# Optimization experiments

Measured on AMD Instinct MI355X. Metric: run time of the kernel, lower is better.

Reference implementation:

```python
import jax, jax.numpy as jnp
import numpy as np

B, K, D, H, A = 8192, 10, 64, 128, 16
E = K * (K - 1)
# lexicographic ordered pairs (i,j), i != j -- matches adj.nonzero() and sorted(Dict.keys())
_PAIRS = np.array([(i, j) for i in range(K) for j in range(K) if i != j], dtype=np.int32)
SRC = jnp.asarray(_PAIRS[:, 0])  # message for edge (i,j) is aggregated at node i (row)
DST = jnp.asarray(_PAIRS[:, 1])


def setup_inputs() -> dict:
    key = jax.random.key(0)
    k1, k2, k3, k4, k5, k6 = jax.random.split(key, 6)
    F = D + H + A  # node MLP input dim
    return {
        "states": jax.random.normal(k1, (B, K, D), jnp.float32),
        "action_vec": jax.random.normal(k2, (B, K, A), jnp.float32),
        # one Linear(2D -> H) per ordered pair, stacked [E, 2D, H]
        "W_edge": jax.random.normal(k3, (E, 2 * D, H), jnp.float32) * (1.0 / np.sqrt(2 * D)),
        "b_edge": jax.random.normal(k4, (E, H), jnp.float32) * 0.01,
        # one Linear(D+H+A -> D) per node, stacked [K, F, D]
        "W_node": jax.random.normal(k5, (K, F, D), jnp.float32) * (1.0 / np.sqrt(F)),
        "b_node": jax.random.normal(k6, (K, D), jnp.float32) * 0.01,
    }


def reference(states, action_vec, W_edge, b_edge, W_node, b_node):
    # states: [B,K,D], action_vec: [B,K,A]
    b, k, d = states.shape
    # gather endpoints per ordered edge: [B,E,2D]
    pair_feat = jnp.concatenate([states[:, SRC, :], states[:, DST, :]], axis=-1)
    # per-edge-type Linear + tanh, batched as one grouped GEMM: [B,E,H]
    msg = jnp.tanh(jnp.einsum('bef,efh->beh', pair_feat, W_edge) + b_edge)
    # unsorted_segment_sum over source node index (row): [B,K,H]
    agg = jnp.zeros((b, k, msg.shape[-1]), msg.dtype).at[:, SRC, :].add(msg)
    # node input: [x, action, agg] -> per-node Linear + tanh: [B,K,D]
    node_in = jnp.concatenate([states, action_vec, agg], axis=-1)
    out = jnp.tanh(jnp.einsum('bkf,kfd->bkd', node_in, W_node) + b_node)
    return out
```

## Files before the change

### kernel.cpp

```cpp
#include <hip/hip_runtime.h>

typedef _Float16 f16;
typedef _Float16 f16x4 __attribute__((ext_vector_type(4)));
typedef _Float16 f16x8 __attribute__((ext_vector_type(8)));
typedef float    f32x4 __attribute__((ext_vector_type(4)));

#define Kn   10
#define En   90
#define BM   128
#define WE_ELEMS (90*128*128)

__device__ __forceinline__ float fast_exp2(float x){
#if __has_builtin(__builtin_amdgcn_exp2f)
    return __builtin_amdgcn_exp2f(x);
#else
    return exp2f(x);
#endif
}
__device__ __forceinline__ float fast_rcp(float x){
#if __has_builtin(__builtin_amdgcn_rcpf)
    return __builtin_amdgcn_rcpf(x);
#else
    return 1.0f/x;
#endif
}
__device__ __forceinline__ float tanh_fast(float x){
    float e = fast_exp2(x * 2.88539008177792681472f);
    return 1.0f - 2.0f * fast_rcp(e + 1.0f);
}

__global__ void we_transpose(const float* __restrict__ We, f16* __restrict__ out){
    int gid = blockIdx.x*256 + threadIdx.x;
    int e  = gid >> 11;
    int r  = gid & 2047;
    int h  = r & 127;
    int f0 = (r >> 7) << 3;
    const float* src = We + e*16384 + h;
    f16x8 v;
    #pragma unroll
    for (int k=0;k<8;k++) v[k] = (f16)src[(f0+k)*128];
    *(f16x8*)(out + e*16384 + h*128 + f0) = v;
}

__global__ void wn_transpose(const float* __restrict__ Wn, f16* __restrict__ out){
    int gid = blockIdx.x*256 + threadIdx.x;
    int k = gid / 14336;
    int r = gid - k*14336;
    int d = r / 224;
    int f = r - d*224;
    float v = (f < 208) ? Wn[k*13312 + f*64 + d] : 0.0f;
    out[gid] = (f16)v;
}

__launch_bounds__(256, 2)
__global__ void gnn_main(const float* __restrict__ states,
                         const float* __restrict__ action,
                         const float* __restrict__ b_edge,
                         const float* __restrict__ b_node,
                         const f16*  __restrict__ We_t,
                         const f16*  __restrict__ Wn_t,
                         float* __restrict__ out)
{
    __shared__ alignas(16) f16 S[9216 + 9216 + 19456];
    f16* sAi = S;
    f16* sAj = S + 9216;
    f16* sWU = S + 18432;

    const int t    = threadIdx.x;
    const int b0   = blockIdx.x * BM;
    const int i    = blockIdx.y;
    const int lane = t & 63;
    const int wid  = t >> 6;
    const int l15  = lane & 15;
    const int q    = lane >> 4;
    const int qo   = q << 3;
    const int wr = (wid >> 1) * 64;
    const int wc = (wid & 1) * 64;

    #pragma unroll
    for (int it=0; it<8; ++it){
        int cid = it*256 + t;
        int row = cid >> 4;
        int c4  = (cid & 15) << 2;
        const float4 v = *(const float4*)(states + (b0+row)*640 + i*64 + c4);
        f16x4 hv; hv[0]=(f16)v.x; hv[1]=(f16)v.y; hv[2]=(f16)v.z; hv[3]=(f16)v.w;
        *(f16x4*)(sAi + row*72 + c4) = hv;
    }

    f32x4 agg[4][4] = {};

    #pragma unroll 1
    for (int et=0; et<9; ++et){
        const int j = et + (et >= i);
        const int e = 9*i + et;

        #pragma unroll
        for (int it=0; it<8; ++it){
            int cid = it*256 + t;
            int row = cid >> 4;
            int c4  = (cid & 15) << 2;
            const float4 v = *(const float4*)(states + (b0+row)*640 + j*64 + c4);
            f16x4 hv; hv[0]=(f16)v.x; hv[1]=(f16)v.y; hv[2]=(f16)v.z; hv[3]=(f16)v.w;
            *(f16x4*)(sAj + row*72 + c4) = hv;
        }
        const f16* wsrc = We_t + e*16384;
        #pragma unroll
        for (int it=0; it<8; ++it){
            int cid = it*256 + t;
            int h   = cid >> 4;
            int c8  = (cid & 15) << 3;
            *(f16x8*)(sWU + h*136 + c8) = *(const f16x8*)(wsrc + h*128 + c8);
        }
        __syncthreads();

        f32x4 msg[4][4] = {};
        #pragma unroll
        for (int ks=0; ks<4; ++ks){
            const f16* ab = (ks<2) ? (sAi + ks*32) : (sAj + (ks-2)*32);
            f16x8 af[4], bf[4];
            #pragma unroll
            for (int rt=0; rt<4; ++rt)
                af[rt] = *(const f16x8*)(ab + (wr + rt*16 + l15)*72 + qo);
            #pragma unroll
            for (int c=0; c<4; ++c)
                bf[c] = *(const f16x8*)(sWU + (wc + c*16 + l15)*136 + ks*32 + qo);
            #pragma unroll
            for (int rt=0; rt<4; ++rt)
                #pragma unroll
                for (int c=0; c<4; ++c)
                    msg[rt][c] = __builtin_amdgcn_mfma_f32_16x16x32_f16(af[rt], bf[c], msg[rt][c], 0,0,0);
        }
        float bias[4];
        #pragma unroll
        for (int c=0;c<4;c++) bias[c] = b_edge[e*128 + wc + c*16 + l15];
        #pragma unroll
        for (int rt=0; rt<4; ++rt)
            #pragma unroll
            for (int c=0;c<4;c++)
                #pragma unroll
                for (int r2=0;r2<4;r2++)
                    agg[rt][c][r2] += tanh_fast(msg[rt][c][r2] + bias[c]);
        __syncthreads();
    }

    #pragma unroll
    for (int rt=0; rt<4; ++rt)
        #pragma unroll
        for (int c=0;c<4;c++)
            #pragma unroll
            for (int r2=0;r2<4;r2++){
                int row = wr + rt*16 + q*4 + r2;
                int col = wc + c*16 + l15;
                sWU[row*152 + col] = (f16)agg[rt][c][r2];
            }
    {
        int row = t >> 1, c0 = 128 + ((t & 1) << 3);
        f16x8 z; 
        #pragma unroll
        for (int k=0;k<8;k++) z[k] = (f16)0.0f;
        *(f16x8*)(sWU + row*152 + c0) = z;
    }
    #pragma unroll
    for (int it=0; it<2; ++it){
        int cid = it*256 + t;
        int row = cid >> 2;
        int c4  = (cid & 3) << 2;
        const float4 v = *(const float4*)(action + (b0+row)*160 + i*16 + c4);
        f16x4 hv; hv[0]=(f16)v.x; hv[1]=(f16)v.y; hv[2]=(f16)v.z; hv[3]=(f16)v.w;
        *(f16x4*)(sAj + row*72 + c4) = hv;
    }
    __syncthreads();

    f32x4 acc[2][4] = {};
    const f16* wn = Wn_t + i*14336;
    #pragma unroll
    for (int ks=0; ks<7; ++ks){
        int kk = ks*32 + qo;
        f16x8 af[2], bf[4];
        #pragma unroll
        for (int rt=0; rt<2; ++rt){
            int row = wid*32 + rt*16 + l15;
            const f16* ap = (kk < 64) ? (sAi + row*72 + kk)
                          : (kk < 80) ? (sAj + row*72 + (kk-64))
                                      : (sWU + row*152 + (kk-80));
            af[rt] = *(const f16x8*)ap;
        }
        #pragma unroll
        for (int c=0;c<4;c++)
            bf[c] = *(const f16x8*)(wn + (c*16 + l15)*224 + kk);
        #pragma unroll
        for (int rt=0; rt<2; ++rt)
            #pragma unroll
            for (int c=0;c<4;c++)
                acc[rt][c] = __builtin_amdgcn_mfma_f32_16x16x32_f16(af[rt], bf[c], acc[rt][c], 0,0,0);
    }
    float bn[4];
    #pragma unroll
    for (int c=0;c<4;c++) bn[c] = b_node[i*64 + c*16 + l15];
    #pragma unroll
    for (int rt=0; rt<2; ++rt)
        #pragma unroll
        for (int c=0;c<4;c++)
            #pragma unroll
            for (int r2=0;r2<4;r2++){
                int row = wid*32 + rt*16 + q*4 + r2;
                int col = c*16 + l15;
                out[((b0+row)*10 + i)*64 + col] = tanh_fast(acc[rt][c][r2] + bn[c]);
            }
}

extern "C" void kernel_launch(void* const* d_in, const int* in_sizes, int n_in,
                              void* d_out, int out_size, void* d_ws, size_t ws_size,
                              hipStream_t stream) {
    const float* states = (const float*)d_in[0];
    const float* action = (const float*)d_in[1];
    const float* W_edge = (const float*)d_in[2];
    const float* b_edge = (const float*)d_in[3];
    const float* W_node = (const float*)d_in[4];
    const float* b_node = (const float*)d_in[5];
    f16* We_t = (f16*)d_ws;
    f16* Wn_t = We_t + WE_ELEMS;

    hipLaunchKernelGGL(we_transpose, dim3(720), dim3(256), 0, stream, W_edge, We_t);
    hipLaunchKernelGGL(wn_transpose, dim3(560), dim3(256), 0, stream, W_node, Wn_t);
    hipLaunchKernelGGL(gnn_main, dim3(8192/BM, Kn), dim3(256), 0, stream,
                       states, action, b_edge, b_node, We_t, Wn_t, (float*)d_out);
}
```

Baseline: 157.7 us.

## Pre-convert inputs to fp16, stream via global_load_lds with swizzled double-buffered LDS

A single prep kernel converts states and action to fp16, pre-swizzles edge and node weights into MFMA fragment order, and pre-scales biases by the tanh exponent constant. The main kernel loads state tiles directly into LDS with global_load_lds, double-buffers the neighbour tile, and uses an XOR swizzle instead of padded rows. Edge weights are read straight from global memory into registers in fragment order, so the weight staging through LDS goes away. The tanh accumulation is rewritten with folded constants, adding +9 at the end. The extra full-array fp16 conversion pass adds memory traffic, and a third occupancy target may add register pressure.

```diff
diff --git a/kernel.cpp b/kernel.cpp
--- a/kernel.cpp
+++ b/kernel.cpp
@@ -5,10 +5,13 @@
 typedef _Float16 f16x8 __attribute__((ext_vector_type(8)));
 typedef float    f32x4 __attribute__((ext_vector_type(4)));
 
-#define Kn   10
-#define En   90
-#define BM   128
-#define WE_ELEMS (90*128*128)
+#define S2C 2.88539008177792681472f
+
+#define OFF_ST16 0u
+#define OFF_AC16 5242880u
+#define OFF_WEF  6553600u
+#define OFF_WNF  8028160u
+#define OFF_BE2  8171520u
 
 __device__ __forceinline__ float fast_exp2(float x){
 #if __has_builtin(__builtin_amdgcn_exp2f)
@@ -24,155 +27,168 @@
     return 1.0f/x;
 #endif
 }
-__device__ __forceinline__ float tanh_fast(float x){
-    float e = fast_exp2(x * 2.88539008177792681472f);
-    return 1.0f - 2.0f * fast_rcp(e + 1.0f);
-}
-
-__global__ void we_transpose(const float* __restrict__ We, f16* __restrict__ out){
-    int gid = blockIdx.x*256 + threadIdx.x;
-    int e  = gid >> 11;
-    int r  = gid & 2047;
-    int h  = r & 127;
-    int f0 = (r >> 7) << 3;
-    const float* src = We + e*16384 + h;
-    f16x8 v;
-    #pragma unroll
-    for (int k=0;k<8;k++) v[k] = (f16)src[(f0+k)*128];
-    *(f16x8*)(out + e*16384 + h*128 + f0) = v;
-}
-
-__global__ void wn_transpose(const float* __restrict__ Wn, f16* __restrict__ out){
-    int gid = blockIdx.x*256 + threadIdx.x;
-    int k = gid / 14336;
-    int r = gid - k*14336;
-    int d = r / 224;
-    int f = r - d*224;
-    float v = (f < 208) ? Wn[k*13312 + f*64 + d] : 0.0f;
-    out[gid] = (f16)v;
-}
-
-__launch_bounds__(256, 2)
-__global__ void gnn_main(const float* __restrict__ states,
-                         const float* __restrict__ action,
-                         const float* __restrict__ b_edge,
-                         const float* __restrict__ b_node,
-                         const f16*  __restrict__ We_t,
-                         const f16*  __restrict__ Wn_t,
-                         float* __restrict__ out)
-{
-    __shared__ alignas(16) f16 S[9216 + 9216 + 19456];
-    f16* sAi = S;
-    f16* sAj = S + 9216;
-    f16* sWU = S + 18432;
-
-    const int t    = threadIdx.x;
-    const int b0   = blockIdx.x * BM;
-    const int i    = blockIdx.y;
-    const int lane = t & 63;
-    const int wid  = t >> 6;
-    const int l15  = lane & 15;
-    const int q    = lane >> 4;
-    const int qo   = q << 3;
-    const int wr = (wid >> 1) * 64;
-    const int wc = (wid & 1) * 64;
-
-    #pragma unroll
-    for (int it=0; it<8; ++it){
-        int cid = it*256 + t;
-        int row = cid >> 4;
-        int c4  = (cid & 15) << 2;
-        const float4 v = *(const float4*)(states + (b0+row)*640 + i*64 + c4);
-        f16x4 hv; hv[0]=(f16)v.x; hv[1]=(f16)v.y; hv[2]=(f16)v.z; hv[3]=(f16)v.w;
-        *(f16x4*)(sAi + row*72 + c4) = hv;
-    }
+
+__device__ __forceinline__ void gl_lds16(const f16* g, f16* l){
+    __builtin_amdgcn_global_load_lds(
+        (const __attribute__((address_space(1))) unsigned int*)g,
+        (__attribute__((address_space(3))) unsigned int*)l, 16, 0, 0);
+}
+
+#define MFMA16(a,b,c) __builtin_amdgcn_mfma_f32_16x16x32_f16(a,b,c,0,0,0)
+
+__global__ void prep(const float* __restrict__ st, const float* __restrict__ ac,
+                     const float* __restrict__ We, const float* __restrict__ be,
+                     const float* __restrict__ Wn, const float* __restrict__ bn,
+                     f16* __restrict__ ws16){
+    const int bid = blockIdx.x, t = threadIdx.x;
+    if (bid < 5120){
+        int g = bid*256 + t;
+        const float4 v = ((const float4*)st)[g];
+        f16x4 h; h[0]=(f16)v.x; h[1]=(f16)v.y; h[2]=(f16)v.z; h[3]=(f16)v.w;
+        *(f16x4*)(ws16 + OFF_ST16 + (size_t)g*4) = h;
+    } else if (bid < 6400){
+        int g = (bid-5120)*256 + t;
+        const float4 v = ((const float4*)ac)[g];
+        f16x4 h; h[0]=(f16)v.x; h[1]=(f16)v.y; h[2]=(f16)v.z; h[3]=(f16)v.w;
+        *(f16x4*)(ws16 + OFF_AC16 + (size_t)g*4) = h;
+    } else if (bid < 7120){
+        int g = (bid-6400)*256 + t;
+        int l = g & 15, q = (g>>4)&3, cg = (g>>6)&7, ks = (g>>9)&3, e = g>>11;
+        const float* src = We + e*16384 + (ks*32 + q*8)*128 + cg*16 + l;
+        f16x8 h;
+        #pragma unroll
+        for (int u=0;u<8;u++) h[u] = (f16)src[u*128];
+        *(f16x8*)(ws16 + OFF_WEF + (size_t)g*8) = h;
+    } else if (bid < 7190){
+        int g = (bid-7120)*256 + t;
+        int l = g&15, q = (g>>4)&3, c = (g>>6)&3, r = g>>8;
+        int ks = r % 7, k = r / 7;
+        f16x8 h;
+        #pragma unroll
+        for (int u=0;u<8;u++){
+            int f = ks*32 + q*8 + u;
+            h[u] = (f < 208) ? (f16)Wn[k*13312 + f*64 + c*16 + l] : (f16)0.0f;
+        }
+        *(f16x8*)(ws16 + OFF_WNF + (size_t)k*14336 + ((ks*4 + c)*64 + q*16 + l)*8) = h;
+    } else {
+        int g = (bid-7190)*256 + t;
+        float* be2 = (float*)(ws16 + OFF_BE2);
+        if (g < 11520)      be2[g] = S2C*be[g];
+        else if (g < 12160) be2[g] = S2C*bn[g-11520];
+    }
+}
+
+__launch_bounds__(256, 3)
+__global__ void gnn_main(const f16* __restrict__ ws16, float* __restrict__ out){
+    const f16* st  = ws16 + OFF_ST16;
+    const f16* ac  = ws16 + OFF_AC16;
+    const f16* Wef = ws16 + OFF_WEF;
+    const f16* Wnf = ws16 + OFF_WNF;
+    const float* be2 = (const float*)(ws16 + OFF_BE2);
+    const float* bn2 = be2 + 11520;
+
+    __shared__ alignas(16) f16 S[26624];
+
+    const int t = threadIdx.x, lane = t&63, wid = t>>6;
+    const int b0 = blockIdx.x*128;
+    const int i  = blockIdx.y;
+    const int l15 = lane&15, q = lane>>4, qo = q<<3;
+    const int wr = (wid>>1)*64, wc = (wid&1)*64;
+    const int lr = lane>>3, lc = lane&7;
+    const int swz = lc ^ (lr&7);
+
+    {
+        const f16* gs = st + (size_t)b0*640 + i*64;
+        #pragma unroll
+        for (int it=0; it<4; ++it){
+            int r0 = (wid*4+it)*8;
+            gl_lds16(gs + (size_t)(r0+lr)*640 + swz*8, S + r0*64);
+        }
+        {
+            int r0 = wid*32; int row = r0 + (lane>>1); int ch = (lane&1) ^ (row&1);
+            gl_lds16(ac + (size_t)(b0+row)*160 + i*16 + ch*8, S + 24576 + r0*16);
+        }
+        int j0 = (i==0) ? 1 : 0;
+        const f16* gj = st + (size_t)b0*640 + j0*64;
+        #pragma unroll
+        for (int it=0; it<4; ++it){
+            int r0 = (wid*4+it)*8;
+            gl_lds16(gj + (size_t)(r0+lr)*640 + swz*8, S + 8192 + r0*64);
+        }
+    }
+    __syncthreads();
 
     f32x4 agg[4][4] = {};
 
     #pragma unroll 1
-    for (int et=0; et<9; ++et){
-        const int j = et + (et >= i);
-        const int e = 9*i + et;
-
-        #pragma unroll
-        for (int it=0; it<8; ++it){
-            int cid = it*256 + t;
-            int row = cid >> 4;
-            int c4  = (cid & 15) << 2;
-            const float4 v = *(const float4*)(states + (b0+row)*640 + j*64 + c4);
-            f16x4 hv; hv[0]=(f16)v.x; hv[1]=(f16)v.y; hv[2]=(f16)v.z; hv[3]=(f16)v.w;
-            *(f16x4*)(sAj + row*72 + c4) = hv;
-        }
-        const f16* wsrc = We_t + e*16384;
-        #pragma unroll
-        for (int it=0; it<8; ++it){
-            int cid = it*256 + t;
-            int h   = cid >> 4;
-            int c8  = (cid & 15) << 3;
-            *(f16x8*)(sWU + h*136 + c8) = *(const f16x8*)(wsrc + h*128 + c8);
+    for (int e=0; e<9; ++e){
+        if (e < 8){
+            int j2 = (e+1) + ((e+1) >= i);
+            const f16* gj = st + (size_t)b0*640 + j2*64;
+            f16* dst = S + 8192 + (((e+1)&1)<<13);
+            #pragma unroll
+            for (int it=0; it<4; ++it){
+                int r0 = (wid*4+it)*8;
+                gl_lds16(gj + (size_t)(r0+lr)*640 + swz*8, dst + r0*64);
+            }
+        }
+        const int bufb  = 8192 + ((e&1)<<13);
+        const int ebase = 9*i + e;
+
+        #pragma unroll
+        for (int h=0; h<2; ++h){
+            f32x4 msg[4][2] = {};
+            #pragma unroll
+            for (int ks=0; ks<4; ++ks){
+                int cg0 = (wid&1)*4 + h*2;
+                const f16* wb = Wef + (size_t)((ebase*4 + ks)*8 + cg0)*512 + lane*8;
+                f16x8 w0 = *(const f16x8*)wb;
+                f16x8 w1 = *(const f16x8*)(wb + 512);
+                int ab = (ks<2) ? 0 : bufb;
+                int ch = (ks&1)*4 + q;
+                f16x8 af[4];
+                #pragma unroll
+                for (int rt=0; rt<4; ++rt){
+                    int row = wr + rt*16 + l15;
+                    af[rt] = *(const f16x8*)(S + ab + row*64 + ((ch ^ (l15&7))<<3));
+                }
+                #pragma unroll
+                for (int rt=0; rt<4; ++rt){
+                    msg[rt][0] = MFMA16(af[rt], w0, msg[rt][0]);
+                    msg[rt][1] = MFMA16(af[rt], w1, msg[rt][1]);
+                }
+            }
+            #pragma unroll
+            for (int c=0; c<2; ++c){
+                float bv = be2[ebase*128 + wc + (h*2+c)*16 + l15];
+                #pragma unroll
+                for (int rt=0; rt<4; ++rt)
+                    #pragma unroll
+                    for (int r2=0; r2<4; ++r2){
+                        float tt = __builtin_fmaf(msg[rt][c][r2], S2C, bv);
+                        float rr = fast_rcp(fast_exp2(tt) + 1.0f);
+                        agg[rt][h*2+c][r2] = __builtin_fmaf(-2.0f, rr, agg[rt][h*2+c][r2]);
+                    }
+            }
         }
         __syncthreads();
-
-        f32x4 msg[4][4] = {};
-        #pragma unroll
-        for (int ks=0; ks<4; ++ks){
-            const f16* ab = (ks<2) ? (sAi + ks*32) : (sAj + (ks-2)*32);
-            f16x8 af[4], bf[4];
-            #pragma unroll
-            for (int rt=0; rt<4; ++rt)
-                af[rt] = *(const f16x8*)(ab + (wr + rt*16 + l15)*72 + qo);
-            #pragma unroll
-            for (int c=0; c<4; ++c)
-                bf[c] = *(const f16x8*)(sWU + (wc + c*16 + l15)*136 + ks*32 + qo);
-            #pragma unroll
-            for (int rt=0; rt<4; ++rt)
-                #pragma unroll
-                for (int c=0; c<4; ++c)
-                    msg[rt][c] = __builtin_amdgcn_mfma_f32_16x16x32_f16(af[rt], bf[c], msg[rt][c], 0,0,0);
-        }
-        float bias[4];
-        #pragma unroll
-        for (int c=0;c<4;c++) bias[c] = b_edge[e*128 + wc + c*16 + l15];
-        #pragma unroll
-        for (int rt=0; rt<4; ++rt)
-            #pragma unroll
-            for (int c=0;c<4;c++)
-                #pragma unroll
-                for (int r2=0;r2<4;r2++)
-                    agg[rt][c][r2] += tanh_fast(msg[rt][c][r2] + bias[c]);
-        __syncthreads();
     }
 
     #pragma unroll
     for (int rt=0; rt<4; ++rt)
         #pragma unroll
-        for (int c=0;c<4;c++)
-            #pragma unroll
-            for (int r2=0;r2<4;r2++){
+        for (int c=0; c<4; ++c)
+            #pragma unroll
+            for (int r2=0; r2<4; ++r2){
                 int row = wr + rt*16 + q*4 + r2;
                 int col = wc + c*16 + l15;
-                sWU[row*152 + col] = (f16)agg[rt][c][r2];
-            }
-    {
-        int row = t >> 1, c0 = 128 + ((t & 1) << 3);
-        f16x8 z; 
-        #pragma unroll
-        for (int k=0;k<8;k++) z[k] = (f16)0.0f;
-        *(f16x8*)(sWU + row*152 + c0) = z;
-    }
-    #pragma unroll
-    for (int it=0; it<2; ++it){
-        int cid = it*256 + t;
-        int row = cid >> 2;
-        int c4  = (cid & 3) << 2;
-        const float4 v = *(const float4*)(action + (b0+row)*160 + i*16 + c4);
-        f16x4 hv; hv[0]=(f16)v.x; hv[1]=(f16)v.y; hv[2]=(f16)v.z; hv[3]=(f16)v.w;
-        *(f16x4*)(sAj + row*72 + c4) = hv;
-    }
+                int ch = (col>>3) ^ (row&7);
+                S[8192 + row*128 + ch*8 + (col&7)] = (f16)(agg[rt][c][r2] + 9.0f);
+            }
     __syncthreads();
 
     f32x4 acc[2][4] = {};
-    const f16* wn = Wn_t + i*14336;
+    const f16* wnb = Wnf + (size_t)i*14336;
     #pragma unroll
     for (int ks=0; ks<7; ++ks){
         int kk = ks*32 + qo;
@@ -180,32 +196,38 @@
         #pragma unroll
         for (int rt=0; rt<2; ++rt){
             int row = wid*32 + rt*16 + l15;
-            const f16* ap = (kk < 64) ? (sAi + row*72 + kk)
-                          : (kk < 80) ? (sAj + row*72 + (kk-64))
-                                      : (sWU + row*152 + (kk-80));
-            af[rt] = *(const f16x8*)ap;
-        }
-        #pragma unroll
-        for (int c=0;c<4;c++)
-            bf[c] = *(const f16x8*)(wn + (c*16 + l15)*224 + kk);
+            f16x8 a;
+            if (kk < 64)       a = *(const f16x8*)(S + row*64  + (((kk>>3)      ^ (l15&7))<<3));
+            else if (kk < 80)  a = *(const f16x8*)(S + 24576 + row*16 + ((((kk-64)>>3) ^ (l15&1))<<3));
+            else if (kk < 208) a = *(const f16x8*)(S + 8192  + row*128 + ((((kk-80)>>3) ^ (l15&7))<<3));
+            else { f16x8 z; 
+                   #pragma unroll
+                   for (int u=0;u<8;u++) z[u]=(f16)0.0f; a = z; }
+            af[rt] = a;
+        }
+        #pragma unroll
+        for (int c=0; c<4; ++c)
+            bf[c] = *(const f16x8*)(wnb + (size_t)((ks*4+c)*64)*8 + lane*8);
         #pragma unroll
         for (int rt=0; rt<2; ++rt)
             #pragma unroll
-            for (int c=0;c<4;c++)
-                acc[rt][c] = __builtin_amdgcn_mfma_f32_16x16x32_f16(af[rt], bf[c], acc[rt][c], 0,0,0);
-    }
-    float bn[4];
-    #pragma unroll
-    for (int c=0;c<4;c++) bn[c] = b_node[i*64 + c*16 + l15];
+            for (int c=0; c<4; ++c)
+                acc[rt][c] = MFMA16(af[rt], bf[c], acc[rt][c]);
+    }
+    float bnv[4];
+    #pragma unroll
+    for (int c=0; c<4; ++c) bnv[c] = bn2[i*64 + c*16 + l15];
     #pragma unroll
     for (int rt=0; rt<2; ++rt)
         #pragma unroll
-        for (int c=0;c<4;c++)
-            #pragma unroll
-            for (int r2=0;r2<4;r2++){
+        for (int c=0; c<4; ++c)
+            #pragma unroll
+            for (int r2=0; r2<4; ++r2){
                 int row = wid*32 + rt*16 + q*4 + r2;
                 int col = c*16 + l15;
-                out[((b0+row)*10 + i)*64 + col] = tanh_fast(acc[rt][c][r2] + bn[c]);
+                float tt = __builtin_fmaf(acc[rt][c][r2], S2C, bnv[c]);
+                float rr = fast_rcp(fast_exp2(tt) + 1.0f);
+                out[((size_t)(b0+row)*10 + i)*64 + col] = __builtin_fmaf(-2.0f, rr, 1.0f);
             }
 }
 
@@ -218,11 +240,10 @@
     const float* b_edge = (const float*)d_in[3];
     const float* W_node = (const float*)d_in[4];
     const float* b_node = (const float*)d_in[5];
-    f16* We_t = (f16*)d_ws;
-    f16* Wn_t = We_t + WE_ELEMS;
-
-    hipLaunchKernelGGL(we_transpose, dim3(720), dim3(256), 0, stream, W_edge, We_t);
-    hipLaunchKernelGGL(wn_transpose, dim3(560), dim3(256), 0, stream, W_node, Wn_t);
-    hipLaunchKernelGGL(gnn_main, dim3(8192/BM, Kn), dim3(256), 0, stream,
-                       states, action, b_edge, b_node, We_t, Wn_t, (float*)d_out);
-}
+    f16* ws16 = (f16*)d_ws;
+
+    hipLaunchKernelGGL(prep, dim3(7238), dim3(256), 0, stream,
+                       states, action, W_edge, b_edge, W_node, b_node, ws16);
+    hipLaunchKernelGGL(gnn_main, dim3(64, 10), dim3(256), 0, stream,
+                       ws16, (float*)d_out);
+}
```

Result: slower. 178.4 us (+13.2%).
